# Optimization experiments

Measured on AMD Instinct MI355X. Metric: run time of the kernel, lower is better.

The kernel has to match this reference:

```python
import jax, jax.numpy as jnp
import numpy as np

VOXEL_SPACING = 1.0

def _laplacian_kernel():
    k = np.zeros((3, 3, 3), dtype=np.float32)
    k[1, 1, 1] = -6.0
    k[0, 1, 1] = k[2, 1, 1] = 1.0
    k[1, 0, 1] = k[1, 2, 1] = 1.0
    k[1, 1, 0] = k[1, 1, 2] = 1.0
    return jnp.asarray(k)[None, None]  # [O=1, I=1, 3, 3, 3]

def setup_inputs() -> dict:
    key = jax.random.key(0)
    k1, k2, k3, k4 = jax.random.split(key, 4)
    shape = (4, 1, 128, 128, 128)
    u = jax.random.uniform(k1, shape, dtype=jnp.float32)
    du_dt = jax.random.normal(k2, shape, dtype=jnp.float32)
    D = jax.random.uniform(k3, shape, dtype=jnp.float32)
    rho = jax.random.uniform(k4, shape, dtype=jnp.float32)
    return {"u": u, "du_dt": du_dt, "D": D, "rho": rho}

def reference(u, du_dt, D, rho):
    kern = _laplacian_kernel()
    # 7-point Laplacian stencil, zero padding (matches F.conv3d padding=1)
    lap_u = jax.lax.conv_general_dilated(
        u, kern,
        window_strides=(1, 1, 1),
        padding=[(1, 1), (1, 1), (1, 1)],
        dimension_numbers=("NCDHW", "OIDHW", "NCDHW"),
    ) / (VOXEL_SPACING ** 2)
    diffusion = D * lap_u
    reaction = rho * u * (1.0 - u)
    residual = du_dt - (diffusion + reaction)
    return jnp.mean(residual ** 2)
```

## Files before the change

kernel.cpp:

```cpp
#include <hip/hip_runtime.h>


#define TOTAL_F4     2097152
#define NUM_BLOCKS   8192
#define INV_N        (1.0f / 8388608.0f)

typedef float floatx4 __attribute__((ext_vector_type(4)));

__device__ __forceinline__ floatx4 load4(const float* p) {
    return *reinterpret_cast<const floatx4*>(p);
}

__global__ __launch_bounds__(256) void fk_loss_kernel(
    const float* __restrict__ u,
    const float* __restrict__ dudt,
    const float* __restrict__ D,
    const float* __restrict__ rho,
    float* __restrict__ partials)
{
    const int t = blockIdx.x * blockDim.x + threadIdx.x;

    const int w4 = t & 31;
    const int h  = (t >> 5) & 127;
    const int d  = (t >> 12) & 127;

    const long base = (long)t * 4;

    const floatx4 c  = load4(u    + base);
    const floatx4 dd = load4(dudt + base);
    const floatx4 Dv = load4(D    + base);
    const floatx4 rv = load4(rho  + base);

    const floatx4 zero = (floatx4)(0.f);

    const float left  = (w4 == 0)  ? 0.f : u[base - 1];
    const float right = (w4 == 31) ? 0.f : u[base + 4];

    const floatx4 hm = (h == 0)   ? zero : load4(u + base - 128);
    const floatx4 hp = (h == 127) ? zero : load4(u + base + 128);

    const floatx4 dm = (d == 0)   ? zero : load4(u + base - 16384);
    const floatx4 dp = (d == 127) ? zero : load4(u + base + 16384);

    float lap[4];
    lap[0] = left + c.y + hm.x + hp.x + dm.x + dp.x - 6.0f * c.x;
    lap[1] = c.x  + c.z + hm.y + hp.y + dm.y + dp.y - 6.0f * c.y;
    lap[2] = c.y  + c.w + hm.z + hp.z + dm.z + dp.z - 6.0f * c.z;
    lap[3] = c.z + right + hm.w + hp.w + dm.w + dp.w - 6.0f * c.w;

    const float cc[4]  = {c.x, c.y, c.z, c.w};
    const float dda[4] = {dd.x, dd.y, dd.z, dd.w};
    const float Da[4]  = {Dv.x, Dv.y, Dv.z, Dv.w};
    const float ra[4]  = {rv.x, rv.y, rv.z, rv.w};

    float partial = 0.f;
#pragma unroll
    for (int i = 0; i < 4; ++i) {
        const float reaction = ra[i] * cc[i] * (1.0f - cc[i]);
        const float residual = dda[i] - (Da[i] * lap[i] + reaction);
        partial += residual * residual;
    }

#pragma unroll
    for (int off = 32; off > 0; off >>= 1)
        partial += __shfl_down(partial, off);

    __shared__ float smem[4];
    const int lane = threadIdx.x & 63;
    const int wid  = threadIdx.x >> 6;
    if (lane == 0) smem[wid] = partial;
    __syncthreads();

    if (threadIdx.x == 0)
        partials[blockIdx.x] = (smem[0] + smem[1]) + (smem[2] + smem[3]);
}

__global__ __launch_bounds__(1024) void fk_reduce_kernel(
    const float* __restrict__ partials, float* __restrict__ out)
{
    float s = 0.f;
#pragma unroll
    for (int i = 0; i < NUM_BLOCKS / 1024; ++i)
        s += partials[threadIdx.x + i * 1024];

#pragma unroll
    for (int off = 32; off > 0; off >>= 1)
        s += __shfl_down(s, off);

    __shared__ float smem[16];
    const int lane = threadIdx.x & 63;
    const int wid  = threadIdx.x >> 6;
    if (lane == 0) smem[wid] = s;
    __syncthreads();

    if (threadIdx.x == 0) {
        float t = 0.f;
#pragma unroll
        for (int i = 0; i < 16; ++i) t += smem[i];
        out[0] = t * INV_N;
    }
}

extern "C" void kernel_launch(void* const* d_in, const int* in_sizes, int n_in,
                              void* d_out, int out_size, void* d_ws, size_t ws_size,
                              hipStream_t stream) {
    const float* u    = (const float*)d_in[0];
    const float* dudt = (const float*)d_in[1];
    const float* D    = (const float*)d_in[2];
    const float* rho  = (const float*)d_in[3];
    float* out      = (float*)d_out;
    float* partials = (float*)d_ws;

    fk_loss_kernel<<<NUM_BLOCKS, 256, 0, stream>>>(u, dudt, D, rho, partials);
    fk_reduce_kernel<<<1, 1024, 0, stream>>>(partials, out);
}
```

Before: 147.4 us.

## Tile stencil into 3D bricks and share neighbour values via LDS

Remaps each block to a 16x8x8 brick of the volume and stores the centre u values in shared memory so interior stencil neighbours come from LDS instead of separate global loads. Only halo faces still read u from global memory. This aims to cut redundant neighbour traffic through the cache hierarchy. In exchange it adds a barrier, divergent halo branches, and narrower 64-byte contiguous rows that may coalesce less efficiently.

```diff
diff --git a/kernel.cpp b/kernel.cpp
--- a/kernel.cpp
+++ b/kernel.cpp
@@ -1,7 +1,6 @@
 #include <hip/hip_runtime.h>
 
 
-#define TOTAL_F4     2097152
 #define NUM_BLOCKS   8192
 #define INV_N        (1.0f / 8388608.0f)
 
@@ -18,29 +17,51 @@
     const float* __restrict__ rho,
     float* __restrict__ partials)
 {
-    const int t = blockIdx.x * blockDim.x + threadIdx.x;
+    const int bid = blockIdx.x;
+    const int wc = bid & 7;
+    const int hc = (bid >> 3) & 15;
+    const int dc = (bid >> 7) & 15;
+    const int n  = bid >> 11;
 
-    const int w4 = t & 31;
-    const int h  = (t >> 5) & 127;
-    const int d  = (t >> 12) & 127;
+    const int tid = threadIdx.x;
+    const int w4 = tid & 3;
+    const int r  = (tid >> 2) & 7;
+    const int dl = tid >> 5;
 
-    const long base = (long)t * 4;
+    const int wf4 = wc * 4 + w4;
+    const int h   = hc * 8 + r;
+    const int d   = dc * 8 + dl;
+
+    const long base = (long)n * 2097152 + (long)d * 16384 + h * 128 + wf4 * 4;
 
     const floatx4 c  = load4(u    + base);
     const floatx4 dd = load4(dudt + base);
     const floatx4 Dv = load4(D    + base);
     const floatx4 rv = load4(rho  + base);
 
+    __shared__ floatx4 us[256];
+    us[tid] = c;
+    __syncthreads();
+
     const floatx4 zero = (floatx4)(0.f);
 
-    const float left  = (w4 == 0)  ? 0.f : u[base - 1];
-    const float right = (w4 == 31) ? 0.f : u[base + 4];
+    floatx4 dm, dp;
+    if (dl > 0)      dm = us[tid - 32];
+    else             dm = (d == 0)   ? zero : load4(u + base - 16384);
+    if (dl < 7)      dp = us[tid + 32];
+    else             dp = (d == 127) ? zero : load4(u + base + 16384);
 
-    const floatx4 hm = (h == 0)   ? zero : load4(u + base - 128);
-    const floatx4 hp = (h == 127) ? zero : load4(u + base + 128);
+    floatx4 hm, hp;
+    if (r > 0)       hm = us[tid - 4];
+    else             hm = (h == 0)   ? zero : load4(u + base - 128);
+    if (r < 7)       hp = us[tid + 4];
+    else             hp = (h == 127) ? zero : load4(u + base + 128);
 
-    const floatx4 dm = (d == 0)   ? zero : load4(u + base - 16384);
-    const floatx4 dp = (d == 127) ? zero : load4(u + base + 16384);
+    float left, right;
+    if (w4 > 0)      left  = us[tid - 1].w;
+    else             left  = (wf4 == 0)  ? 0.f : u[base - 1];
+    if (w4 < 3)      right = us[tid + 1].x;
+    else             right = (wf4 == 31) ? 0.f : u[base + 4];
 
     float lap[4];
     lap[0] = left + c.y + hm.x + hp.x + dm.x + dp.x - 6.0f * c.x;
@@ -66,13 +87,13 @@
         partial += __shfl_down(partial, off);
 
     __shared__ float smem[4];
-    const int lane = threadIdx.x & 63;
-    const int wid  = threadIdx.x >> 6;
+    const int lane = tid & 63;
+    const int wid  = tid >> 6;
     if (lane == 0) smem[wid] = partial;
     __syncthreads();
 
-    if (threadIdx.x == 0)
-        partials[blockIdx.x] = (smem[0] + smem[1]) + (smem[2] + smem[3]);
+    if (tid == 0)
+        partials[bid] = (smem[0] + smem[1]) + (smem[2] + smem[3]);
 }
 
 __global__ __launch_bounds__(1024) void fk_reduce_kernel(
```

Result: slower. 164.1 us (+11.3%).
